# Kernel optimization log

Hardware: AMD Instinct MI355X
Metric: run time of the kernel (lower is better)

## Reference

```python
import jax, jax.numpy as jnp
import numpy as np

INPUT_SIZE = 128
UNITS = 128          # hidden_size * 2 in the torch module
BATCH = 128
SEQ = 1024
ODE_UNFOLDS = 4
EPS_ODE = 1e-8
EPS_LN = 1e-5


def _layernorm(x, g, b):
    m = jnp.mean(x, axis=-1, keepdims=True)
    v = jnp.mean((x - m) ** 2, axis=-1, keepdims=True)
    return (x - m) * jax.lax.rsqrt(v + EPS_LN) * g + b


def setup_inputs() -> dict:
    key = jax.random.key(0)
    ks = jax.random.split(key, 16)
    u = lambda k, shp, lo, hi: jax.random.uniform(k, shp, jnp.float32, lo, hi)
    D, U = INPUT_SIZE, UNITS
    return {
        "x": jax.random.normal(ks[0], (BATCH, SEQ, D), jnp.float32),
        "pre_W": jax.random.normal(ks[1], (D, D), jnp.float32) * (1.0 / np.sqrt(D)),
        "pre_b": jnp.zeros((D,), jnp.float32),
        "pre_ln_g": jnp.ones((D,), jnp.float32),
        "pre_ln_b": jnp.zeros((D,), jnp.float32),
        # ncps LTCCell parameter init ranges
        "gleak": u(ks[2], (U,), 0.001, 1.0),
        "vleak": u(ks[3], (U,), -0.2, 0.2),
        "cm": u(ks[4], (U,), 0.4, 0.6),
        "sigma": u(ks[5], (U, U), 3.0, 8.0),
        "mu": u(ks[6], (U, U), 0.3, 0.8),
        "w": u(ks[7], (U, U), 0.001, 1.0),
        "erev": jnp.sign(jax.random.normal(ks[8], (U, U))).astype(jnp.float32),
        "sensory_sigma": u(ks[9], (D, U), 3.0, 8.0),
        "sensory_mu": u(ks[10], (D, U), 0.3, 0.8),
        "sensory_w": u(ks[11], (D, U), 0.001, 1.0),
        "sensory_erev": jnp.sign(jax.random.normal(ks[12], (D, U))).astype(jnp.float32),
        "input_w": jnp.ones((D,), jnp.float32),
        "input_b": jnp.zeros((D,), jnp.float32),
        "output_w": jnp.ones((U,), jnp.float32),
        "output_b": jnp.zeros((U,), jnp.float32),
        "ltc_ln_g": jnp.ones((U,), jnp.float32),
        "ltc_ln_b": jnp.zeros((U,), jnp.float32),
        # 5 heads of 3 units fused: [attitude|velocity|position|gyro_bias|accel_bias]
        "head_W": jax.random.normal(ks[13], (15, U), jnp.float32) * (1.0 / np.sqrt(U)),
        "head_b": jnp.zeros((15,), jnp.float32),
    }


def _ltc_last(h, gleak, vleak, cm, sigma, mu, w, erev, sensory_sigma, sensory_mu,
              sensory_w, sensory_erev, input_w, input_b, output_w, output_b):
    # h: [B, T, D]. Fully-connected ncps LTC cell, implicit param constraints
    # (softplus on gleak/cm/w/sensory_w), ode_unfolds=4, elapsed_time=1.0.
    gleak_p = jax.nn.softplus(gleak)                 # [U]
    cm_t = jax.nn.softplus(cm) * ODE_UNFOLDS         # cm / (1.0 / ode_unfolds)
    w_p = jax.nn.softplus(w)                         # [U, U]
    sw_p = jax.nn.softplus(sensory_w)                # [D, U]

    def step(v, inp):
        inp = inp * input_w + input_b                # affine input mapping, [B, D]
        # sensory synapse activation: [B, D, U]
        s_act = sw_p * jax.nn.sigmoid(sensory_sigma * (inp[:, :, None] - sensory_mu))
        w_num_s = jnp.sum(s_act * sensory_erev, axis=1)   # [B, U]
        w_den_s = jnp.sum(s_act, axis=1)                  # [B, U]
        for _ in range(ODE_UNFOLDS):
            w_act = w_p * jax.nn.sigmoid(sigma * (v[:, :, None] - mu))  # [B, U, U]
            w_num = jnp.sum(w_act * erev, axis=1) + w_num_s
            w_den = jnp.sum(w_act, axis=1) + w_den_s
            v = (cm_t * v + gleak_p * vleak + w_num) / (cm_t + gleak_p + w_den + EPS_ODE)
        return v, None

    v0 = jnp.zeros((h.shape[0], gleak.shape[0]), h.dtype)
    v_last, _ = jax.lax.scan(jax.checkpoint(step), v0, jnp.swapaxes(h, 0, 1))
    # affine output mapping; only the last timestep is used downstream
    return v_last * output_w + output_b


def reference(x, pre_W, pre_b, pre_ln_g, pre_ln_b, gleak, vleak, cm, sigma, mu, w, erev,
              sensory_sigma, sensory_mu, sensory_w, sensory_erev, input_w, input_b,
              output_w, output_b, ltc_ln_g, ltc_ln_b, head_W, head_b):
    h = x @ pre_W.T + pre_b                 # pre_process Linear
    h = _layernorm(h, pre_ln_g, pre_ln_b)   # pre_norm; dropout = identity (eval)
    last = _ltc_last(h, gleak, vleak, cm, sigma, mu, w, erev, sensory_sigma,
                     sensory_mu, sensory_w, sensory_erev, input_w, input_b,
                     output_w, output_b)    # ltc_out[:, -1, :]
    out = _layernorm(last, ltc_ln_g, ltc_ln_b)
    # concatenated heads: [attitude|velocity|position|gyro_bias|accel_bias] -> [B, 15]
    return out @ head_W.T + head_b
```

## Files before the change

### kernel.cpp

```cpp
#include <hip/hip_runtime.h>

#define LOG2E 1.4426950408889634f

typedef float f32x2 __attribute__((ext_vector_type(2)));

__device__ __forceinline__ unsigned short f2bf(float f) {
  unsigned u = __float_as_uint(f);
  u += 0x7FFFu + ((u >> 16) & 1u);
  return (unsigned short)(u >> 16);
}
__device__ __forceinline__ unsigned pk2(float a, float b) {
  return (unsigned)f2bf(a) | ((unsigned)f2bf(b) << 16);
}
__device__ __forceinline__ float bl16(unsigned u) { return __uint_as_float(u << 16); }
__device__ __forceinline__ float bh16(unsigned u) { return __uint_as_float(u & 0xFFFF0000u); }

__device__ __forceinline__ void lds_barrier() {
  asm volatile("s_waitcnt lgkmcnt(0)" ::: "memory");
  __builtin_amdgcn_s_barrier();
}

__device__ __forceinline__ float dpp_xor1_add(float x) {
  return x + __int_as_float(__builtin_amdgcn_update_dpp(
      0, __float_as_int(x), 0xB1, 0xF, 0xF, true));
}
__device__ __forceinline__ float dpp_xor2_add(float x) {
  return x + __int_as_float(__builtin_amdgcn_update_dpp(
      0, __float_as_int(x), 0x4E, 0xF, 0xF, true));
}
__device__ __forceinline__ float dpp_xor7_add(float x) {
  return x + __int_as_float(__builtin_amdgcn_update_dpp(
      0, __float_as_int(x), 0x141, 0xF, 0xF, true));
}
__device__ __forceinline__ float red8(float x) {
  x = dpp_xor1_add(x);
  x = dpp_xor2_add(x);
  x = dpp_xor7_add(x);
  return x;
}

__device__ __forceinline__ void sigacc3(float c2, float a2, float we, float vi,
                                        float& an, float& ad) {
  float t = fmaf(-a2, vi, c2);
  float e = __builtin_amdgcn_exp2f(t);
  float r = __builtin_amdgcn_rcpf(1.0f + e);
  an = fmaf(we, r, an);
  ad = fmaf(fabsf(we), r, ad);
}

__global__ __launch_bounds__(256) void prep_kernel(
    const float* __restrict__ sigma, const float* __restrict__ mu,
    const float* __restrict__ w,     const float* __restrict__ erev,
    const float* __restrict__ ss,    const float* __restrict__ smu,
    const float* __restrict__ sw,    const float* __restrict__ serev,
    const float* __restrict__ iw,    const float* __restrict__ ib,
    const float* __restrict__ gleak, const float* __restrict__ vleak,
    const float* __restrict__ cm,
    float* __restrict__ C2r, float* __restrict__ A2r, float* __restrict__ WEr,
    float* __restrict__ C2s, float* __restrict__ A2s, float* __restrict__ WEs,
    float* __restrict__ vecs)
{
  int gid = blockIdx.x * 256 + threadIdx.x;
  if (gid < 16384) {
    int i = gid >> 7, j = gid & 127;
    int idx = j * 128 + i;
    float a2 = sigma[gid] * LOG2E;
    float c2 = a2 * mu[gid];
    float sp = log1pf(expf(w[gid]));
    float we = sp * erev[gid];
    C2r[idx] = c2; A2r[idx] = a2; WEr[idx] = we;
  } else if (gid < 32768) {
    int e = gid - 16384;
    int i = e >> 7, j = e & 127;
    int idx = j * 128 + i;
    float a2 = ss[e] * iw[i] * LOG2E;
    float c2 = ss[e] * (smu[e] - ib[i]) * LOG2E;
    float sp = log1pf(expf(sw[e]));
    float we = sp * serev[e];
    C2s[idx] = c2; A2s[idx] = a2; WEs[idx] = we;
  } else if (gid < 32896) {
    int jj = gid - 32768;
    float gp = log1pf(expf(gleak[jj]));
    vecs[jj]       = log1pf(expf(cm[jj])) * 4.0f;
    vecs[128 + jj] = gp;
    vecs[256 + jj] = gp * vleak[jj];
  }
}

__global__ __launch_bounds__(256) void stage_a(
    const float* __restrict__ x, const float* __restrict__ W,
    const float* __restrict__ pb, const float* __restrict__ lg,
    const float* __restrict__ lb, uint4* __restrict__ hout)
{
  extern __shared__ char smem[];
  float* Wt = (float*)smem;
  float* xs = Wt + 128 * 132;
  const int tid = threadIdx.x;

  #pragma unroll
  for (int ii = 0; ii < 16; ++ii) {
    int f = tid + (ii << 8);
    int jrow = f >> 5, kq = f & 31;
    float4 wv = ((const float4*)W)[f];
    float* wd = Wt + jrow;
    wd[(4 * kq + 0) * 132] = wv.x;
    wd[(4 * kq + 1) * 132] = wv.y;
    wd[(4 * kq + 2) * 132] = wv.z;
    wd[(4 * kq + 3) * 132] = wv.w;
  }
  const size_t R0 = (size_t)blockIdx.x << 5;
  const float4* xg = (const float4*)(x + (R0 << 7));
  #pragma unroll
  for (int ii = 0; ii < 4; ++ii) {
    int f = tid + (ii << 8);
    int r = f >> 5, kq = f & 31;
    *(float4*)(xs + r * 132 + (kq << 2)) = xg[f];
  }
  __syncthreads();

  const int tr = tid >> 4, tc = tid & 15;
  const int r0 = tr << 1, j0 = tc << 3;
  float a0[8], a1[8];
  #pragma unroll
  for (int c = 0; c < 8; ++c) { a0[c] = 0.f; a1[c] = 0.f; }
  const float* xr0 = xs + r0 * 132;
  const float* xr1 = xs + (r0 + 1) * 132;
  const float* wc = Wt + j0;
  for (int k = 0; k < 128; k += 4) {
    float4 xa = *(const float4*)(xr0 + k);
    float4 xb = *(const float4*)(xr1 + k);
    #pragma unroll
    for (int s = 0; s < 4; ++s) {
      float4 w0 = *(const float4*)(wc + (k + s) * 132);
      float4 w1 = *(const float4*)(wc + (k + s) * 132 + 4);
      float xav = s == 0 ? xa.x : s == 1 ? xa.y : s == 2 ? xa.z : xa.w;
      float xbv = s == 0 ? xb.x : s == 1 ? xb.y : s == 2 ? xb.z : xb.w;
      a0[0] = fmaf(xav, w0.x, a0[0]); a0[1] = fmaf(xav, w0.y, a0[1]);
      a0[2] = fmaf(xav, w0.z, a0[2]); a0[3] = fmaf(xav, w0.w, a0[3]);
      a0[4] = fmaf(xav, w1.x, a0[4]); a0[5] = fmaf(xav, w1.y, a0[5]);
      a0[6] = fmaf(xav, w1.z, a0[6]); a0[7] = fmaf(xav, w1.w, a0[7]);
      a1[0] = fmaf(xbv, w0.x, a1[0]); a1[1] = fmaf(xbv, w0.y, a1[1]);
      a1[2] = fmaf(xbv, w0.z, a1[2]); a1[3] = fmaf(xbv, w0.w, a1[3]);
      a1[4] = fmaf(xbv, w1.x, a1[4]); a1[5] = fmaf(xbv, w1.y, a1[5]);
      a1[6] = fmaf(xbv, w1.z, a1[6]); a1[7] = fmaf(xbv, w1.w, a1[7]);
    }
  }
  float4 pb0 = *(const float4*)(pb + j0);
  float4 pb1 = *(const float4*)(pb + j0 + 4);
  a0[0] += pb0.x; a0[1] += pb0.y; a0[2] += pb0.z; a0[3] += pb0.w;
  a0[4] += pb1.x; a0[5] += pb1.y; a0[6] += pb1.z; a0[7] += pb1.w;
  a1[0] += pb0.x; a1[1] += pb0.y; a1[2] += pb0.z; a1[3] += pb0.w;
  a1[4] += pb1.x; a1[5] += pb1.y; a1[6] += pb1.z; a1[7] += pb1.w;
  float s0 = 0, q0 = 0, s1 = 0, q1 = 0;
  #pragma unroll
  for (int c = 0; c < 8; ++c) {
    s0 += a0[c]; q0 = fmaf(a0[c], a0[c], q0);
    s1 += a1[c]; q1 = fmaf(a1[c], a1[c], q1);
  }
  #pragma unroll
  for (int m = 1; m < 16; m <<= 1) {
    s0 += __shfl_xor(s0, m, 64); q0 += __shfl_xor(q0, m, 64);
    s1 += __shfl_xor(s1, m, 64); q1 += __shfl_xor(q1, m, 64);
  }
  float mu0 = s0 * (1.f / 128.f), mu1 = s1 * (1.f / 128.f);
  float rs0 = rsqrtf(fmaf(-mu0, mu0, q0 * (1.f / 128.f)) + 1e-5f);
  float rs1 = rsqrtf(fmaf(-mu1, mu1, q1 * (1.f / 128.f)) + 1e-5f);
  float4 g0 = *(const float4*)(lg + j0), g1 = *(const float4*)(lg + j0 + 4);
  float4 b0 = *(const float4*)(lb + j0), b1 = *(const float4*)(lb + j0 + 4);
  float n0[8], n1[8];
  const float* gv = (const float*)&g0; const float* bv = (const float*)&b0;
  #pragma unroll
  for (int c = 0; c < 4; ++c) {
    n0[c] = fmaf((a0[c] - mu0) * rs0, gv[c], bv[c]);
    n1[c] = fmaf((a1[c] - mu1) * rs1, gv[c], bv[c]);
  }
  const float* gv1 = (const float*)&g1; const float* bv1 = (const float*)&b1;
  #pragma unroll
  for (int c = 0; c < 4; ++c) {
    n0[4 + c] = fmaf((a0[4 + c] - mu0) * rs0, gv1[c], bv1[c]);
    n1[4 + c] = fmaf((a1[4 + c] - mu1) * rs1, gv1[c], bv1[c]);
  }
  uint4 o0, o1;
  o0.x = pk2(n0[0], n0[1]); o0.y = pk2(n0[2], n0[3]);
  o0.z = pk2(n0[4], n0[5]); o0.w = pk2(n0[6], n0[7]);
  o1.x = pk2(n1[0], n1[1]); o1.y = pk2(n1[2], n1[3]);
  o1.z = pk2(n1[4], n1[5]); o1.w = pk2(n1[6], n1[7]);
  hout[(R0 + r0) * 16 + tc] = o0;
  hout[(R0 + r0 + 1) * 16 + tc] = o1;
}

__global__ __launch_bounds__(1024, 4) void sensory_kernel(
    const float* __restrict__ C2, const float* __restrict__ A2,
    const float* __restrict__ WE,
    const uint4* __restrict__ hbf, unsigned* __restrict__ ndg)
{
  const int tid = threadIdx.x;
  const int lane = tid & 63, wv = tid >> 6;
  const int iq = lane & 7, jj = lane >> 3;
  const int j = wv * 8 + jj;

  float c2s[16], a2s[16], wes[16];
  const int pbase = j * 128 + iq * 16;
  #pragma unroll
  for (int k = 0; k < 16; ++k) {
    c2s[k] = C2[pbase + k];
    a2s[k] = A2[pbase + k];
    wes[k] = WE[pbase + k];
  }

  const int p0 = blockIdx.x << 9;
  uint4 hc0 = hbf[((size_t)p0 << 4) + iq * 2];
  uint4 hc1 = hbf[((size_t)p0 << 4) + iq * 2 + 1];

  for (int q = 0; q < 512; ++q) {
    const int p = p0 + q;
    const int pn = p0 + (q + 1 < 512 ? q + 1 : q);
    uint4 hn0 = hbf[((size_t)pn << 4) + iq * 2];
    uint4 hn1 = hbf[((size_t)pn << 4) + iq * 2 + 1];

    float hv[16];
    hv[0] = bl16(hc0.x);  hv[1] = bh16(hc0.x);
    hv[2] = bl16(hc0.y);  hv[3] = bh16(hc0.y);
    hv[4] = bl16(hc0.z);  hv[5] = bh16(hc0.z);
    hv[6] = bl16(hc0.w);  hv[7] = bh16(hc0.w);
    hv[8] = bl16(hc1.x);  hv[9] = bh16(hc1.x);
    hv[10] = bl16(hc1.y); hv[11] = bh16(hc1.y);
    hv[12] = bl16(hc1.z); hv[13] = bh16(hc1.z);
    hv[14] = bl16(hc1.w); hv[15] = bh16(hc1.w);

    float an = 0.f, ad = 0.f;
    #pragma unroll
    for (int k = 0; k < 16; ++k)
      sigacc3(c2s[k], a2s[k], wes[k], hv[k], an, ad);

    an = red8(an);
    ad = red8(ad);
    if (iq == 0) ndg[((size_t)p << 7) + j] = pk2(an, ad);
    hc0 = hn0; hc1 = hn1;
  }
}

__global__ __launch_bounds__(1024, 4) void ltc_scan(
    const float* __restrict__ C2, const float* __restrict__ A2,
    const float* __restrict__ WE,
    const float* __restrict__ vecs, const unsigned* __restrict__ ndg,
    const float* __restrict__ ow, const float* __restrict__ ob,
    const float* __restrict__ lng, const float* __restrict__ lnb,
    const float* __restrict__ hW, const float* __restrict__ hb,
    float* __restrict__ out)
{
  __shared__ float vbuf[2][8 * 36];
  __shared__ float ov[128], lnv[128], mv[2];

  const int tid = threadIdx.x;
  const int lane = tid & 63, wv = tid >> 6;
  const int iq = lane & 7, jj = lane >> 3;
  const int j = wv * 8 + jj;
  const int b = blockIdx.x;
  const int vpos_j = ((j >> 4) * 36) + (j & 15);

  float c2s[16], a2s[16], wes[16];
  const int pbase = j * 128 + iq * 16;
  #pragma unroll
  for (int k = 0; k < 16; ++k) {
    c2s[k] = C2[pbase + k];
    a2s[k] = A2[pbase + k];
    wes[k] = WE[pbase + k];
  }
  const float cmtj = vecs[j];
  const float gdj  = vecs[128 + j];
  const float gnj  = vecs[256 + j];
  const float cgd  = cmtj + gdj + 1e-8f;
  float vj = 0.f;
  if (tid < 128) vbuf[0][((tid >> 4) * 36) + (tid & 15)] = 0.f;
  __syncthreads();

  const size_t ndbase = ((size_t)b << 17) + j;
  unsigned ndc = ndg[ndbase];
  for (int t = 0; t < 1024; ++t) {
    const int tn = (t + 1 < 1024) ? t + 1 : 1023;
    unsigned ndn = ndg[ndbase + ((size_t)tn << 7)];
    const float snum = bl16(ndc), sden = bh16(ndc);
    #pragma unroll
    for (int u = 0; u < 4; ++u) {
      const float* vc = vbuf[u & 1] + iq * 36;
      float an = 0.f, ad = 0.f;
      #pragma unroll
      for (int c = 0; c < 4; ++c) {
        float4 vv = *(const float4*)(vc + 4 * c);
        sigacc3(c2s[4 * c + 0], a2s[4 * c + 0], wes[4 * c + 0], vv.x, an, ad);
        sigacc3(c2s[4 * c + 1], a2s[4 * c + 1], wes[4 * c + 1], vv.y, an, ad);
        sigacc3(c2s[4 * c + 2], a2s[4 * c + 2], wes[4 * c + 2], vv.z, an, ad);
        sigacc3(c2s[4 * c + 3], a2s[4 * c + 3], wes[4 * c + 3], vv.w, an, ad);
      }
      an = red8(an);
      ad = red8(ad);
      float num = an + snum;
      float den = ad + sden;
      float vnew = (fmaf(cmtj, vj, gnj) + num) *
                   __builtin_amdgcn_rcpf(cgd + den);
      if (iq == 0) vbuf[(u & 1) ^ 1][vpos_j] = vnew;
      vj = vnew;
      lds_barrier();
    }
    ndc = ndn;
  }

  __syncthreads();
  if (tid < 128)
    ov[tid] = fmaf(vbuf[0][((tid >> 4) * 36) + (tid & 15)], ow[tid], ob[tid]);
  __syncthreads();
  if (tid < 64) {
    float a = ov[tid], c = ov[tid + 64];
    float s = a + c, s2 = fmaf(a, a, c * c);
    #pragma unroll
    for (int m = 1; m < 64; m <<= 1) {
      s += __shfl_xor(s, m, 64);
      s2 += __shfl_xor(s2, m, 64);
    }
    if (tid == 0) {
      float mean = s * (1.f / 128.f);
      float var = s2 * (1.f / 128.f) - mean * mean;
      mv[0] = mean;
      mv[1] = rsqrtf(var + 1e-5f);
    }
  }
  __syncthreads();
  if (tid < 128) lnv[tid] = fmaf((ov[tid] - mv[0]) * mv[1], lng[tid], lnb[tid]);
  __syncthreads();
  if (tid < 15) {
    float acc = hb[tid];
    const float* wr = hW + tid * 128;
    #pragma unroll
    for (int k = 0; k < 128; k += 4) {
      float4 wvv = *(const float4*)(wr + k);
      acc = fmaf(wvv.x, lnv[k], acc);
      acc = fmaf(wvv.y, lnv[k + 1], acc);
      acc = fmaf(wvv.z, lnv[k + 2], acc);
      acc = fmaf(wvv.w, lnv[k + 3], acc);
    }
    out[b * 15 + tid] = acc;
  }
}

extern "C" void kernel_launch(void* const* d_in, const int* in_sizes, int n_in,
                              void* d_out, int out_size, void* d_ws, size_t ws_size,
                              hipStream_t stream) {
  const float* x      = (const float*)d_in[0];
  const float* pre_W  = (const float*)d_in[1];
  const float* pre_b  = (const float*)d_in[2];
  const float* plg    = (const float*)d_in[3];
  const float* plb    = (const float*)d_in[4];
  const float* gleak  = (const float*)d_in[5];
  const float* vleak  = (const float*)d_in[6];
  const float* cm     = (const float*)d_in[7];
  const float* sigma  = (const float*)d_in[8];
  const float* mu     = (const float*)d_in[9];
  const float* w      = (const float*)d_in[10];
  const float* erev   = (const float*)d_in[11];
  const float* ss     = (const float*)d_in[12];
  const float* smu    = (const float*)d_in[13];
  const float* sw     = (const float*)d_in[14];
  const float* serev  = (const float*)d_in[15];
  const float* iw     = (const float*)d_in[16];
  const float* ib     = (const float*)d_in[17];
  const float* ow     = (const float*)d_in[18];
  const float* ob     = (const float*)d_in[19];
  const float* lng    = (const float*)d_in[20];
  const float* lnb    = (const float*)d_in[21];
  const float* hW     = (const float*)d_in[22];
  const float* hb     = (const float*)d_in[23];
  float* out = (float*)d_out;

  char* ws = (char*)d_ws;
  float* C2r = (float*)(ws + 0 * 65536);
  float* A2r = (float*)(ws + 1 * 65536);
  float* WEr = (float*)(ws + 2 * 65536);
  float* C2s = (float*)(ws + 3 * 65536);
  float* A2s = (float*)(ws + 4 * 65536);
  float* WEs = (float*)(ws + 5 * 65536);
  float* vecs   = (float*)(ws + 6 * 65536);
  uint4* hbf    = (uint4*)(ws + 1048576);
  unsigned* ndg = (unsigned*)(ws + 1048576 + 33554432);

  prep_kernel<<<129, 256, 0, stream>>>(sigma, mu, w, erev, ss, smu, sw, serev,
                                       iw, ib, gleak, vleak, cm,
                                       C2r, A2r, WEr, C2s, A2s, WEs, vecs);
  stage_a<<<4096, 256, 84480, stream>>>(x, pre_W, pre_b, plg, plb, hbf);
  sensory_kernel<<<256, 1024, 0, stream>>>(C2s, A2s, WEs, hbf, ndg);
  ltc_scan<<<128, 1024, 0, stream>>>(C2r, A2r, WEr, vecs, ndg,
                                     ow, ob, lng, lnb, hW, hb, out);
}
```

Baseline: 4.997 ms.

## Stage recurrent sigmoid parameters in swizzled LDS instead of registers

The prep kernel now writes the recurrent (c2, a2) pairs as one interleaved float2 image, XOR-swizzled per neuron to avoid LDS bank conflicts. The scan kernel copies that 128 KB image into dynamic shared memory and reads it with float4 loads inside the unfold loop. Only the weights stay in registers. This frees about 32 VGPRs per thread and lowers register pressure in the 1024-thread block, but it adds two LDS reads per four synapses on the serial, latency-bound critical path.

```diff
diff --git a/kernel.cpp b/kernel.cpp
--- a/kernel.cpp
+++ b/kernel.cpp
@@ -1,8 +1,6 @@
 #include <hip/hip_runtime.h>
 
 #define LOG2E 1.4426950408889634f
-
-typedef float f32x2 __attribute__((ext_vector_type(2)));
 
 __device__ __forceinline__ unsigned short f2bf(float f) {
   unsigned u = __float_as_uint(f);
@@ -37,15 +35,6 @@
   x = dpp_xor2_add(x);
   x = dpp_xor7_add(x);
   return x;
-}
-
-__device__ __forceinline__ void sigacc3(float c2, float a2, float we, float vi,
-                                        float& an, float& ad) {
-  float t = fmaf(-a2, vi, c2);
-  float e = __builtin_amdgcn_exp2f(t);
-  float r = __builtin_amdgcn_rcpf(1.0f + e);
-  an = fmaf(we, r, an);
-  ad = fmaf(fabsf(we), r, ad);
 }
 
 __global__ __launch_bounds__(256) void prep_kernel(
@@ -56,19 +45,21 @@
     const float* __restrict__ iw,    const float* __restrict__ ib,
     const float* __restrict__ gleak, const float* __restrict__ vleak,
     const float* __restrict__ cm,
-    float* __restrict__ C2r, float* __restrict__ A2r, float* __restrict__ WEr,
+    float2* __restrict__ Pimg, float* __restrict__ WEr,
     float* __restrict__ C2s, float* __restrict__ A2s, float* __restrict__ WEs,
     float* __restrict__ vecs)
 {
   int gid = blockIdx.x * 256 + threadIdx.x;
   if (gid < 16384) {
     int i = gid >> 7, j = gid & 127;
-    int idx = j * 128 + i;
     float a2 = sigma[gid] * LOG2E;
     float c2 = a2 * mu[gid];
     float sp = log1pf(expf(w[gid]));
     float we = sp * erev[gid];
-    C2r[idx] = c2; A2r[idx] = a2; WEr[idx] = we;
+    int iq = i >> 4, k = i & 15, c = k >> 1, h = k & 1, jj = j & 7;
+    int idx8 = j * 128 + iq * 16 + ((c ^ jj) << 1) + h;
+    Pimg[idx8] = make_float2(c2, a2);
+    WEr[j * 128 + i] = we;
   } else if (gid < 32768) {
     int e = gid - 16384;
     int i = e >> 7, j = e & 127;
@@ -230,8 +221,13 @@
 
     float an = 0.f, ad = 0.f;
     #pragma unroll
-    for (int k = 0; k < 16; ++k)
-      sigacc3(c2s[k], a2s[k], wes[k], hv[k], an, ad);
+    for (int k = 0; k < 16; ++k) {
+      float t = fmaf(-a2s[k], hv[k], c2s[k]);
+      float e = __builtin_amdgcn_exp2f(t);
+      float r = __builtin_amdgcn_rcpf(1.0f + e);
+      an = fmaf(wes[k], r, an);
+      ad = fmaf(fabsf(wes[k]), r, ad);
+    }
 
     an = red8(an);
     ad = red8(ad);
@@ -241,40 +237,52 @@
 }
 
 __global__ __launch_bounds__(1024, 4) void ltc_scan(
-    const float* __restrict__ C2, const float* __restrict__ A2,
-    const float* __restrict__ WE,
+    const float2* __restrict__ Pimg, const float* __restrict__ WEr,
     const float* __restrict__ vecs, const unsigned* __restrict__ ndg,
     const float* __restrict__ ow, const float* __restrict__ ob,
     const float* __restrict__ lng, const float* __restrict__ lnb,
     const float* __restrict__ hW, const float* __restrict__ hb,
     float* __restrict__ out)
 {
-  __shared__ float vbuf[2][8 * 36];
-  __shared__ float ov[128], lnv[128], mv[2];
+  extern __shared__ char smem[];
+  char* Plds  = smem;
+  float* vbuf0 = (float*)(smem + 131072);
+  float* vbuf1 = vbuf0 + 288;
+  float* ov    = vbuf1 + 288;
+  float* lnv   = ov + 128;
+  float* mv    = lnv + 128;
 
   const int tid = threadIdx.x;
   const int lane = tid & 63, wv = tid >> 6;
-  const int iq = lane & 7, jj = lane >> 3;
-  const int j = wv * 8 + jj;
+  const int iq = lane & 7, jj0 = lane >> 3;
+  const int j = wv * 8 + jj0;
+  const int jj = j & 7;
   const int b = blockIdx.x;
   const int vpos_j = ((j >> 4) * 36) + (j & 15);
 
-  float c2s[16], a2s[16], wes[16];
-  const int pbase = j * 128 + iq * 16;
-  #pragma unroll
-  for (int k = 0; k < 16; ++k) {
-    c2s[k] = C2[pbase + k];
-    a2s[k] = A2[pbase + k];
-    wes[k] = WE[pbase + k];
+  {
+    const float4* img4 = (const float4*)Pimg;
+    float4* dst4 = (float4*)Plds;
+    #pragma unroll
+    for (int it = 0; it < 8; ++it) {
+      int idx = tid + (it << 10);
+      dst4[idx] = img4[idx];
+    }
+  }
+  float4 wq[4];
+  {
+    const float4* wp = (const float4*)(WEr + j * 128 + iq * 16);
+    wq[0] = wp[0]; wq[1] = wp[1]; wq[2] = wp[2]; wq[3] = wp[3];
   }
   const float cmtj = vecs[j];
   const float gdj  = vecs[128 + j];
   const float gnj  = vecs[256 + j];
   const float cgd  = cmtj + gdj + 1e-8f;
   float vj = 0.f;
-  if (tid < 128) vbuf[0][((tid >> 4) * 36) + (tid & 15)] = 0.f;
-  __syncthreads();
-
+  if (tid < 128) vbuf0[((tid >> 4) * 36) + (tid & 15)] = 0.f;
+  __syncthreads();
+
+  const char* pbase = Plds + j * 1024 + iq * 128;
   const size_t ndbase = ((size_t)b << 17) + j;
   unsigned ndc = ndg[ndbase];
   for (int t = 0; t < 1024; ++t) {
@@ -283,15 +291,25 @@
     const float snum = bl16(ndc), sden = bh16(ndc);
     #pragma unroll
     for (int u = 0; u < 4; ++u) {
-      const float* vc = vbuf[u & 1] + iq * 36;
+      const float* vc = (u & 1 ? vbuf1 : vbuf0) + iq * 36;
       float an = 0.f, ad = 0.f;
       #pragma unroll
-      for (int c = 0; c < 4; ++c) {
-        float4 vv = *(const float4*)(vc + 4 * c);
-        sigacc3(c2s[4 * c + 0], a2s[4 * c + 0], wes[4 * c + 0], vv.x, an, ad);
-        sigacc3(c2s[4 * c + 1], a2s[4 * c + 1], wes[4 * c + 1], vv.y, an, ad);
-        sigacc3(c2s[4 * c + 2], a2s[4 * c + 2], wes[4 * c + 2], vv.z, an, ad);
-        sigacc3(c2s[4 * c + 3], a2s[4 * c + 3], wes[4 * c + 3], vv.w, an, ad);
+      for (int cq = 0; cq < 4; ++cq) {
+        float4 vv = *(const float4*)(vc + 4 * cq);
+        float4 pA = *(const float4*)(pbase + (((2 * cq)     ^ jj) << 4));
+        float4 pB = *(const float4*)(pbase + (((2 * cq + 1) ^ jj) << 4));
+        float w0 = cq == 0 ? wq[0].x : cq == 1 ? wq[1].x : cq == 2 ? wq[2].x : wq[3].x;
+        float w1 = cq == 0 ? wq[0].y : cq == 1 ? wq[1].y : cq == 2 ? wq[2].y : wq[3].y;
+        float w2 = cq == 0 ? wq[0].z : cq == 1 ? wq[1].z : cq == 2 ? wq[2].z : wq[3].z;
+        float w3 = cq == 0 ? wq[0].w : cq == 1 ? wq[1].w : cq == 2 ? wq[2].w : wq[3].w;
+        float r0 = __builtin_amdgcn_rcpf(1.0f + __builtin_amdgcn_exp2f(fmaf(-pA.y, vv.x, pA.x)));
+        float r1 = __builtin_amdgcn_rcpf(1.0f + __builtin_amdgcn_exp2f(fmaf(-pA.w, vv.y, pA.z)));
+        float r2 = __builtin_amdgcn_rcpf(1.0f + __builtin_amdgcn_exp2f(fmaf(-pB.y, vv.z, pB.x)));
+        float r3 = __builtin_amdgcn_rcpf(1.0f + __builtin_amdgcn_exp2f(fmaf(-pB.w, vv.w, pB.z)));
+        an = fmaf(w0, r0, an); ad = fmaf(fabsf(w0), r0, ad);
+        an = fmaf(w1, r1, an); ad = fmaf(fabsf(w1), r1, ad);
+        an = fmaf(w2, r2, an); ad = fmaf(fabsf(w2), r2, ad);
+        an = fmaf(w3, r3, an); ad = fmaf(fabsf(w3), r3, ad);
       }
       an = red8(an);
       ad = red8(ad);
@@ -299,7 +317,7 @@
       float den = ad + sden;
       float vnew = (fmaf(cmtj, vj, gnj) + num) *
                    __builtin_amdgcn_rcpf(cgd + den);
-      if (iq == 0) vbuf[(u & 1) ^ 1][vpos_j] = vnew;
+      if (iq == 0) (u & 1 ? vbuf0 : vbuf1)[vpos_j] = vnew;
       vj = vnew;
       lds_barrier();
     }
@@ -308,7 +326,7 @@
 
   __syncthreads();
   if (tid < 128)
-    ov[tid] = fmaf(vbuf[0][((tid >> 4) * 36) + (tid & 15)], ow[tid], ob[tid]);
+    ov[tid] = fmaf(vbuf0[((tid >> 4) * 36) + (tid & 15)], ow[tid], ob[tid]);
   __syncthreads();
   if (tid < 64) {
     float a = ov[tid], c = ov[tid + 64];
@@ -373,21 +391,20 @@
   float* out = (float*)d_out;
 
   char* ws = (char*)d_ws;
-  float* C2r = (float*)(ws + 0 * 65536);
-  float* A2r = (float*)(ws + 1 * 65536);
-  float* WEr = (float*)(ws + 2 * 65536);
-  float* C2s = (float*)(ws + 3 * 65536);
-  float* A2s = (float*)(ws + 4 * 65536);
-  float* WEs = (float*)(ws + 5 * 65536);
-  float* vecs   = (float*)(ws + 6 * 65536);
-  uint4* hbf    = (uint4*)(ws + 1048576);
+  float2* Pimg = (float2*)(ws + 0);
+  float* WEr   = (float*)(ws + 131072);
+  float* C2s   = (float*)(ws + 196608);
+  float* A2s   = (float*)(ws + 262144);
+  float* WEs   = (float*)(ws + 327680);
+  float* vecs  = (float*)(ws + 393216);
+  uint4* hbf   = (uint4*)(ws + 1048576);
   unsigned* ndg = (unsigned*)(ws + 1048576 + 33554432);
 
   prep_kernel<<<129, 256, 0, stream>>>(sigma, mu, w, erev, ss, smu, sw, serev,
                                        iw, ib, gleak, vleak, cm,
-                                       C2r, A2r, WEr, C2s, A2s, WEs, vecs);
+                                       Pimg, WEr, C2s, A2s, WEs, vecs);
   stage_a<<<4096, 256, 84480, stream>>>(x, pre_W, pre_b, plg, plb, hbf);
   sensory_kernel<<<256, 1024, 0, stream>>>(C2s, A2s, WEs, hbf, ndg);
-  ltc_scan<<<128, 1024, 0, stream>>>(C2r, A2r, WEr, vecs, ndg,
-                                     ow, ob, lng, lnb, hW, hb, out);
-}
+  ltc_scan<<<128, 1024, 134480, stream>>>(Pimg, WEr, vecs, ndg,
+                                          ow, ob, lng, lnb, hW, hb, out);
+}
```

After: 5.197 ms. 4.0% more time.
